# Performance work log

Measured on AMD Instinct MI355X. Metric: run time of the kernel, lower is better.

The kernel has to match this reference:

```python
import jax, jax.numpy as jnp
import numpy as np

N, D, H, K, L, C = 65536, 512, 256, 16, 3, 64  # n_support, embed_dim, D//2, max_clusters, num_levels, n_classes
EPS = 1e-5


def setup_inputs() -> dict:
    key = jax.random.key(0)
    ks = jax.random.split(key, 18)
    s = 0.02
    inp = {
        "support_features": jax.random.normal(ks[0], (N, D), jnp.float32),
        "support_labels": jax.random.randint(ks[1], (N,), 0, C),
        # cluster heads (per level): Linear(D,H) -> ReLU -> Linear(H,K) -> Softmax
        "ch_w1": jax.random.normal(ks[2], (L, D, H), jnp.float32) * s,
        "ch_b1": jnp.zeros((L, H), jnp.float32),
        "ch_w2": jax.random.normal(ks[3], (L, H, K), jnp.float32) * s,
        "ch_b2": jnp.zeros((L, K), jnp.float32),
        # prototype refiners (per level): Linear(D,D) -> LayerNorm -> ReLU -> Linear(D,D)
        "ref_w1": jax.random.normal(ks[4], (L, D, D), jnp.float32) * s,
        "ref_b1": jnp.zeros((L, D), jnp.float32),
        "ln_g": jnp.ones((L, D), jnp.float32),
        "ln_b": jnp.zeros((L, D), jnp.float32),
        "ref_w2": jax.random.normal(ks[5], (L, D, D), jnp.float32) * s,
        "ref_b2": jnp.zeros((L, D), jnp.float32),
        # hierarchy combiner: Linear(L*D, D) -> ReLU -> Linear(D, D)
        "comb_w1": jax.random.normal(ks[6], (L * D, D), jnp.float32) * s,
        "comb_b1": jnp.zeros((D,), jnp.float32),
        "comb_w2": jax.random.normal(ks[7], (D, D), jnp.float32) * s,
        "comb_b2": jnp.zeros((D,), jnp.float32),
    }
    return inp


def _layernorm(x, g, b):
    m = x.mean(-1, keepdims=True)
    v = ((x - m) ** 2).mean(-1, keepdims=True)
    return (x - m) * jax.lax.rsqrt(v + EPS) * g + b


def reference(support_features, support_labels, ch_w1, ch_b1, ch_w2, ch_b2,
              ref_w1, ref_b1, ln_g, ln_b, ref_w2, ref_b2,
              comb_w1, comb_b1, comb_w2, comb_b2):
    current = support_features  # [N, D]; per-class offsets applied via label gather
    level_protos = []
    for l in range(L):
        # cluster head; softmax omitted since argmax is softmax-invariant
        logits = jax.nn.relu(current @ ch_w1[l] + ch_b1[l]) @ ch_w2[l] + ch_b2[l]  # [N, K]
        assign = jnp.argmax(logits, axis=-1)  # [N]
        seg = support_labels * K + assign  # combined (class, cluster) segment id
        sums = jax.ops.segment_sum(current, seg, num_segments=C * K)  # [C*K, D]
        cnt = jax.ops.segment_sum(jnp.ones((N,), current.dtype), seg, num_segments=C * K)
        means = sums / jnp.maximum(cnt, 1.0)[:, None]  # empty clusters -> 0, masked below
        h = means @ ref_w1[l] + ref_b1[l]
        h = jax.nn.relu(_layernorm(h, ln_g[l], ln_b[l]))
        refined = (h @ ref_w2[l] + ref_b2[l]).reshape(C, K, D)
        ne = (cnt.reshape(C, K) > 0).astype(current.dtype)  # non-empty cluster mask
        lp = (refined * ne[..., None]).sum(1) / ne.sum(1)[:, None]  # [C, D] mean over non-empty
        level_protos.append(lp)
        current = current + lp[support_labels]
    combined = jnp.concatenate(level_protos, axis=-1)  # [C, L*D]
    protos = jax.nn.relu(combined @ comb_w1 + comb_b1) @ comb_w2 + comb_b2  # [C, D]
    return protos
```

## Files before the change

kernel.cpp:

```cpp
#include <hip/hip_runtime.h>

#define NPTS 65536
#define DIM  512
#define HID  256
#define KCL  16
#define NLVL 3
#define NCLS 64
#define NSEG (NCLS*KCL)
#define EPSF 1e-5f

typedef __bf16 bf16_t;
typedef bf16_t bf16x4 __attribute__((ext_vector_type(4)));
typedef bf16_t bf16x8 __attribute__((ext_vector_type(8)));
typedef float  f32x4  __attribute__((ext_vector_type(4)));

#define LDA 40
#define LDH2 68

__global__ __launch_bounds__(256) void wsplit_kernel(
    const float* __restrict__ w1, bf16_t* __restrict__ hiT, bf16_t* __restrict__ loT)
{
  int gid = blockIdx.x * 256 + threadIdx.x;
  int n = gid >> 9, k = gid & 511;
  int l = n >> 8, j = n & 255;
  float v = w1[l*DIM*HID + k*HID + j];
  bf16_t h = (bf16_t)v;
  hiT[gid] = h;
  loT[gid] = (bf16_t)(v - (float)h);
}

__global__ __launch_bounds__(256) void wsplit2_kernel(
    const float* __restrict__ w1, const float* __restrict__ w2,
    bf16_t* __restrict__ h1, bf16_t* __restrict__ l1,
    bf16_t* __restrict__ h2, bf16_t* __restrict__ l2)
{
  const int per = NLVL*DIM*DIM;
  int gid = blockIdx.x * 256 + threadIdx.x;
  const float* w = (gid < per) ? w1 : w2;
  bf16_t* hh = (gid < per) ? h1 : h2;
  bf16_t* ll = (gid < per) ? l1 : l2;
  int g2 = (gid < per) ? gid : gid - per;
  int n512 = g2 >> 9, k = g2 & 511;
  int l = n512 >> 9, n = n512 & 511;
  float v = w[(size_t)l*DIM*DIM + (size_t)k*DIM + n];
  bf16_t h = (bf16_t)v;
  hh[g2] = h;
  ll[g2] = (bf16_t)(v - (float)h);
}

__global__ __launch_bounds__(256) void wsplitW2_kernel(
    const float* __restrict__ w2, bf16_t* __restrict__ hiT, bf16_t* __restrict__ loT)
{
  int gid = blockIdx.x * 256 + threadIdx.x;
  int l = gid >> 12, rem = gid & 4095;
  int k2 = rem >> 8, k = rem & 255;
  float v = w2[(size_t)l*HID*KCL + k*KCL + k2];
  bf16_t h = (bf16_t)v;
  hiT[gid] = h;
  loT[gid] = (bf16_t)(v - (float)h);
}

__global__ __launch_bounds__(512, 4) void gemmassign_kernel(
    const float* __restrict__ feat,
    const bf16_t* __restrict__ BhiT, const bf16_t* __restrict__ BloT,
    const bf16_t* __restrict__ w2hT, const bf16_t* __restrict__ w2lT,
    const float* __restrict__ offsrc, int ldo,
    const int* __restrict__ labels,
    const float* __restrict__ pb2,
    int* __restrict__ asg, int* __restrict__ cnt)
{
  __shared__ __align__(16) unsigned char SMraw[768*LDA*2];
  __shared__ int labs[128];
  bf16_t* SM  = (bf16_t*)SMraw;
  bf16_t* Ahi = SM;
  bf16_t* Alo = SM + 128*LDA;
  bf16_t* Bhi = SM + 256*LDA;
  bf16_t* Blo = SM + 512*LDA;

  const int t = threadIdx.x;
  const int row0 = blockIdx.x * 128;
  const int w = t >> 6, lane = t & 63;
  const int wm = w & 1, wn = w >> 1;
  const int fm = lane & 15, fq = lane >> 4;

  if (t < 128) labs[t] = labels[row0 + t];
  const float pv = pb2[fm];

  f32x4 acc[4][4];
  #pragma unroll
  for (int i = 0; i < 4; i++)
    #pragma unroll
    for (int j = 0; j < 4; j++)
      #pragma unroll
      for (int r = 0; r < 4; r++) acc[i][j][r] = 0.f;

  for (int kc = 0; kc < DIM; kc += 32) {
    __syncthreads();
    #pragma unroll
    for (int p = 0; p < 2; p++) {
      int idx = t + 512*p;
      int r = idx >> 3, c = idx & 7;
      float4 v = *(const float4*)&feat[(size_t)(row0 + r)*DIM + kc + c*4];
      bf16x4 hi, lo;
      hi[0] = (bf16_t)v.x; lo[0] = (bf16_t)(v.x - (float)hi[0]);
      hi[1] = (bf16_t)v.y; lo[1] = (bf16_t)(v.y - (float)hi[1]);
      hi[2] = (bf16_t)v.z; lo[2] = (bf16_t)(v.z - (float)hi[2]);
      hi[3] = (bf16_t)v.w; lo[3] = (bf16_t)(v.w - (float)hi[3]);
      *(bf16x4*)&Ahi[r*LDA + c*4] = hi;
      *(bf16x4*)&Alo[r*LDA + c*4] = lo;
    }
    #pragma unroll
    for (int p = 0; p < 2; p++) {
      int idx = t + 512*p;
      int n = idx >> 2, c = idx & 3;
      *(bf16x8*)&Bhi[n*LDA + c*8] = *(const bf16x8*)&BhiT[(size_t)n*DIM + kc + c*8];
      *(bf16x8*)&Blo[n*LDA + c*8] = *(const bf16x8*)&BloT[(size_t)n*DIM + kc + c*8];
    }
    __syncthreads();

    bf16x8 ah[4], al[4], bh[4], bl[4];
    #pragma unroll
    for (int mt = 0; mt < 4; mt++) {
      int rr = (wm*64 + mt*16 + fm)*LDA + fq*8;
      ah[mt] = *(bf16x8*)&Ahi[rr];
      al[mt] = *(bf16x8*)&Alo[rr];
    }
    #pragma unroll
    for (int nt = 0; nt < 4; nt++) {
      int rr = (wn*64 + nt*16 + fm)*LDA + fq*8;
      bh[nt] = *(bf16x8*)&Bhi[rr];
      bl[nt] = *(bf16x8*)&Blo[rr];
    }
    #pragma unroll
    for (int mt = 0; mt < 4; mt++)
      #pragma unroll
      for (int nt = 0; nt < 4; nt++) {
        acc[mt][nt] = __builtin_amdgcn_mfma_f32_16x16x32_bf16(ah[mt], bh[nt], acc[mt][nt], 0, 0, 0);
        acc[mt][nt] = __builtin_amdgcn_mfma_f32_16x16x32_bf16(ah[mt], bl[nt], acc[mt][nt], 0, 0, 0);
        acc[mt][nt] = __builtin_amdgcn_mfma_f32_16x16x32_bf16(al[mt], bh[nt], acc[mt][nt], 0, 0, 0);
      }
  }

  __syncthreads();
  float* hS = (float*)SMraw;

  f32x4 lg = {0.f, 0.f, 0.f, 0.f};

  #pragma unroll
  for (int q = 0; q < 4; q++) {
    if (wn == q) {
      #pragma unroll
      for (int nt = 0; nt < 4; nt++) {
        int colq = nt*16 + fm;
        int colg = q*64 + colq;
        #pragma unroll
        for (int mt = 0; mt < 4; mt++)
          #pragma unroll
          for (int r = 0; r < 4; r++) {
            int row = wm*64 + mt*16 + fq*4 + r;
            float hv = fmaxf(acc[mt][nt][r] +
                             offsrc[(size_t)labs[row]*ldo + colg], 0.f);
            hS[row*LDH2 + colq] = hv;
          }
      }
    }
    __syncthreads();

    #pragma unroll
    for (int s = 0; s < 2; s++) {
      int kb = s*32 + fq*8;
      f32x4 a0 = *(f32x4*)&hS[(w*16 + fm)*LDH2 + kb];
      f32x4 a1 = *(f32x4*)&hS[(w*16 + fm)*LDH2 + kb + 4];
      bf16x8 ahf, alf;
      #pragma unroll
      for (int j = 0; j < 4; j++) {
        bf16_t h0 = (bf16_t)a0[j]; ahf[j]   = h0; alf[j]   = (bf16_t)(a0[j] - (float)h0);
        bf16_t h1 = (bf16_t)a1[j]; ahf[4+j] = h1; alf[4+j] = (bf16_t)(a1[j] - (float)h1);
      }
      bf16x8 bhf = *(const bf16x8*)&w2hT[fm*HID + q*64 + kb];
      bf16x8 blf = *(const bf16x8*)&w2lT[fm*HID + q*64 + kb];
      lg = __builtin_amdgcn_mfma_f32_16x16x32_bf16(ahf, bhf, lg, 0, 0, 0);
      lg = __builtin_amdgcn_mfma_f32_16x16x32_bf16(ahf, blf, lg, 0, 0, 0);
      lg = __builtin_amdgcn_mfma_f32_16x16x32_bf16(alf, bhf, lg, 0, 0, 0);
    }
    __syncthreads();
  }

  #pragma unroll
  for (int r = 0; r < 4; r++) {
    float v = lg[r] + pv;
    int idx = fm;
    #pragma unroll
    for (int ofs = 8; ofs > 0; ofs >>= 1) {
      float ov = __shfl_xor(v, ofs, 16);
      int   oi = __shfl_xor(idx, ofs, 16);
      if (ov > v || (ov == v && oi < idx)) { v = ov; idx = oi; }
    }
    if (fm == 0) {
      int rloc = w*16 + fq*4 + r;
      asg[row0 + rloc] = idx;
      atomicAdd(&cnt[labs[rloc]*KCL + idx], 1);
    }
  }
}

__global__ __launch_bounds__(256) void gemm64_kernel(
    const float* __restrict__ Asrc,
    const bf16_t* __restrict__ BhiT, const bf16_t* __restrict__ BloT,
    float* __restrict__ C, int mode,
    const int* __restrict__ cnt, const float* __restrict__ off,
    const float* __restrict__ b1, const float* __restrict__ g,
    const float* __restrict__ bb,
    const float* __restrict__ mS, const float* __restrict__ rS)
{
  __shared__ __align__(16) bf16_t Ahi[64*LDA];
  __shared__ __align__(16) bf16_t Alo[64*LDA];
  __shared__ __align__(16) bf16_t Bhi[64*LDA];
  __shared__ __align__(16) bf16_t Blo[64*LDA];
  __shared__ float rm[64], rr_[64];

  const int t = threadIdx.x;
  const int row0 = blockIdx.x * 64, col0 = blockIdx.y * 64;
  const int w = t >> 6, lane = t & 63;
  const int wm = w & 1, wn = w >> 1;
  const int fm = lane & 15, fq = lane >> 4;

  if (t < 64) {
    if (mode == 1) {
      int n = cnt[row0 + t];
      rm[t] = (float)n;
      rr_[t] = 1.f / fmaxf((float)n, 1.f);
    } else {
      rm[t] = mS[row0 + t];
      rr_[t] = rS[row0 + t];
    }
  }

  f32x4 acc[2][2];
  #pragma unroll
  for (int i = 0; i < 2; i++)
    #pragma unroll
    for (int j = 0; j < 2; j++)
      #pragma unroll
      for (int r = 0; r < 4; r++) acc[i][j][r] = 0.f;

  for (int kc = 0; kc < DIM; kc += 32) {
    __syncthreads();
    #pragma unroll
    for (int p = 0; p < 2; p++) {
      int idx = t + 256*p;
      int r = idx >> 3, c = idx & 7;
      float4 v = *(const float4*)&Asrc[(size_t)(row0 + r)*DIM + kc + c*4];
      if (mode == 1) {
        int cls = (row0 + r) >> 4;
        float4 o = *(const float4*)&off[(size_t)cls*DIM + kc + c*4];
        float n = rm[r], inv = rr_[r];
        v.x = (v.x + n*o.x) * inv; v.y = (v.y + n*o.y) * inv;
        v.z = (v.z + n*o.z) * inv; v.w = (v.w + n*o.w) * inv;
      } else {
        float4 B1 = *(const float4*)&b1[kc + c*4];
        float4 G4 = *(const float4*)&g[kc + c*4];
        float4 BB = *(const float4*)&bb[kc + c*4];
        float m = rm[r], rs = rr_[r];
        v.x = fmaxf((v.x + B1.x - m)*rs*G4.x + BB.x, 0.f);
        v.y = fmaxf((v.y + B1.y - m)*rs*G4.y + BB.y, 0.f);
        v.z = fmaxf((v.z + B1.z - m)*rs*G4.z + BB.z, 0.f);
        v.w = fmaxf((v.w + B1.w - m)*rs*G4.w + BB.w, 0.f);
      }
      bf16x4 hi, lo;
      hi[0] = (bf16_t)v.x; lo[0] = (bf16_t)(v.x - (float)hi[0]);
      hi[1] = (bf16_t)v.y; lo[1] = (bf16_t)(v.y - (float)hi[1]);
      hi[2] = (bf16_t)v.z; lo[2] = (bf16_t)(v.z - (float)hi[2]);
      hi[3] = (bf16_t)v.w; lo[3] = (bf16_t)(v.w - (float)hi[3]);
      *(bf16x4*)&Ahi[r*LDA + c*4] = hi;
      *(bf16x4*)&Alo[r*LDA + c*4] = lo;
    }
    {
      int n = t >> 2, kof = (t & 3)*8;
      *(bf16x8*)&Bhi[n*LDA + kof] = *(const bf16x8*)&BhiT[(size_t)(col0 + n)*DIM + kc + kof];
      *(bf16x8*)&Blo[n*LDA + kof] = *(const bf16x8*)&BloT[(size_t)(col0 + n)*DIM + kc + kof];
    }
    __syncthreads();

    bf16x8 ah[2], al[2], bh[2], bl[2];
    #pragma unroll
    for (int mt = 0; mt < 2; mt++) {
      int idx = (wm*32 + mt*16 + fm)*LDA + fq*8;
      ah[mt] = *(bf16x8*)&Ahi[idx];
      al[mt] = *(bf16x8*)&Alo[idx];
    }
    #pragma unroll
    for (int nt = 0; nt < 2; nt++) {
      int idx = (wn*32 + nt*16 + fm)*LDA + fq*8;
      bh[nt] = *(bf16x8*)&Bhi[idx];
      bl[nt] = *(bf16x8*)&Blo[idx];
    }
    #pragma unroll
    for (int mt = 0; mt < 2; mt++)
      #pragma unroll
      for (int nt = 0; nt < 2; nt++) {
        acc[mt][nt] = __builtin_amdgcn_mfma_f32_16x16x32_bf16(ah[mt], bh[nt], acc[mt][nt], 0, 0, 0);
        acc[mt][nt] = __builtin_amdgcn_mfma_f32_16x16x32_bf16(ah[mt], bl[nt], acc[mt][nt], 0, 0, 0);
        acc[mt][nt] = __builtin_amdgcn_mfma_f32_16x16x32_bf16(al[mt], bh[nt], acc[mt][nt], 0, 0, 0);
        acc[mt][nt] = __builtin_amdgcn_mfma_f32_16x16x32_bf16(al[mt], bl[nt], acc[mt][nt], 0, 0, 0);
      }
  }

  #pragma unroll
  for (int mt = 0; mt < 2; mt++)
    #pragma unroll
    for (int nt = 0; nt < 2; nt++) {
      int col = col0 + wn*32 + nt*16 + fm;
      int rowb = row0 + wm*32 + mt*16 + fq*4;
      #pragma unroll
      for (int r = 0; r < 4; r++)
        C[(size_t)(rowb + r)*DIM + col] = acc[mt][nt][r];
    }
}

__global__ __launch_bounds__(256) void lnstats_kernel(
    const float* __restrict__ Y1, const float* __restrict__ b1,
    float* __restrict__ mS, float* __restrict__ rS)
{
  int r = blockIdx.x, t = threadIdx.x;
  float x0 = Y1[(size_t)r*DIM + t]       + b1[t];
  float x1 = Y1[(size_t)r*DIM + t + 256] + b1[t + 256];
  float s1 = x0 + x1, s2 = x0*x0 + x1*x1;
  #pragma unroll
  for (int ofs = 32; ofs > 0; ofs >>= 1) {
    s1 += __shfl_xor(s1, ofs);
    s2 += __shfl_xor(s2, ofs);
  }
  __shared__ float r1[4], r2[4];
  int lane = t & 63, w = t >> 6;
  if (lane == 0) { r1[w] = s1; r2[w] = s2; }
  __syncthreads();
  if (t == 0) {
    s1 = r1[0] + r1[1] + r1[2] + r1[3];
    s2 = r2[0] + r2[1] + r2[2] + r2[3];
    float m = s1 * (1.f/512.f);
    float var = s2 * (1.f/512.f) - m*m;
    mS[r] = m;
    rS[r] = rsqrtf(var + EPSF);
  }
}

__global__ __launch_bounds__(256) void protoOffgemm_kernel(
    const float* __restrict__ Y2, const float* __restrict__ b2,
    const int* __restrict__ cnt, float* __restrict__ off, float* __restrict__ lp_out,
    const float* __restrict__ w1next, const float* __restrict__ b1next,
    float* __restrict__ offW1b)
{
  __shared__ float offs[DIM];
  int c = blockIdx.x, t = threadIdx.x;
  int nes = 0;
  #pragma unroll
  for (int k = 0; k < KCL; k++) nes += (cnt[c*KCL + k] > 0);
  float inv = 1.f / (float)nes;
  #pragma unroll
  for (int h = 0; h < 2; h++) {
    int d = t + h*256;
    float s = 0.f;
    #pragma unroll
    for (int k = 0; k < KCL; k++)
      if (cnt[c*KCL + k] > 0) s += Y2[(size_t)(c*KCL + k)*DIM + d];
    float lp = s * inv + b2[d];
    lp_out[c*DIM + d] = lp;
    float on = off[c*DIM + d] + lp;
    off[c*DIM + d] = on;
    offs[d] = on;
  }
  if (w1next == nullptr) return;
  __syncthreads();
  float a = 0.f;
  #pragma unroll 4
  for (int d = 0; d < DIM; d++)
    a = fmaf(offs[d], w1next[d*HID + t], a);
  offW1b[c*HID + t] = a + b1next[t];
}

__global__ void scan_kernel(const int* __restrict__ cnt, int* __restrict__ seg_st,
                            int* __restrict__ cursor)
{
  int t = threadIdx.x;
  int4 v = *(const int4*)&cnt[t*4];
  int a0 = v.x, a1 = v.x + v.y, a2 = a1 + v.z, tot = a2 + v.w;
  int lane = t & 63, w = t >> 6;
  int sc = tot;
  #pragma unroll
  for (int ofs = 1; ofs < 64; ofs <<= 1) {
    int u = __shfl_up(sc, ofs);
    if (lane >= ofs) sc += u;
  }
  __shared__ int wt[4];
  if (lane == 63) wt[w] = sc;
  __syncthreads();
  int base = 0;
  #pragma unroll
  for (int i = 0; i < 4; i++) if (i < w) base += wt[i];
  int excl = base + sc - tot;
  seg_st[t*4 + 1] = excl + a0;
  seg_st[t*4 + 2] = excl + a1;
  seg_st[t*4 + 3] = excl + a2;
  seg_st[t*4 + 4] = excl + tot;
  if (t == 0) seg_st[0] = 0;
  int4 cur = {excl, excl + a0, excl + a1, excl + a2};
  *(int4*)&cursor[t*4] = cur;
}

__global__ __launch_bounds__(256) void scatter_kernel(
    const int* __restrict__ labels, const int* __restrict__ asg,
    int* __restrict__ cursor, int* __restrict__ rowlist, int* __restrict__ seglist)
{
  int i = blockIdx.x * 256 + threadIdx.x;
  int seg = labels[i]*KCL + asg[i];
  int pos = atomicAdd(&cursor[seg], 1);
  rowlist[pos] = i;
  seglist[pos] = seg;
}

__global__ __launch_bounds__(256) void means3_kernel(
    const float* __restrict__ feat, const int* __restrict__ rowlist,
    const int* __restrict__ seglist, float* __restrict__ sums)
{
  __shared__ int rows[64];
  __shared__ int segs[65];
  int t = threadIdx.x;
  int i0 = blockIdx.x * 64;
  int col = blockIdx.y * 256 + t;
  if (t < 64) { rows[t] = rowlist[i0 + t]; segs[t] = seglist[i0 + t]; }
  if (t == 64) segs[64] = -1;
  __syncthreads();
  float acc = 0.f;
  for (int base = 0; base < 64; base += 16) {
    float v[16];
    #pragma unroll
    for (int j = 0; j < 16; j++)
      v[j] = feat[(size_t)rows[base + j]*DIM + col];
    #pragma unroll
    for (int j = 0; j < 16; j++) {
      acc += v[j];
      if (segs[base + j] != segs[base + j + 1]) {
        atomicAdd(&sums[(size_t)segs[base + j]*DIM + col], acc);
        acc = 0.f;
      }
    }
  }
}

__global__ __launch_bounds__(256) void fgemm1_kernel(
    const float* __restrict__ lp_all, const float* __restrict__ cw1,
    float* __restrict__ Hacc)
{
  __shared__ float As[64*132];
  __shared__ float Ws[128*64];
  int t = threadIdx.x;
  int nc = blockIdx.x * 64, kc = blockIdx.y * 128;

  #pragma unroll
  for (int p = 0; p < 8; p++) {
    int i = t + 256*p;
    int m = i >> 5, k0 = (i & 31) << 2;
    int k = kc + k0;
    int l = k >> 9, d = k & 511;
    *(float4*)&As[m*132 + k0] = *(const float4*)&lp_all[(size_t)(l*NCLS + m)*DIM + d];
  }
  #pragma unroll
  for (int p = 0; p < 8; p++) {
    int i = t + 256*p;
    int k = i >> 4, n0 = (i & 15) << 2;
    *(float4*)&Ws[k*64 + n0] = *(const float4*)&cw1[(size_t)(kc + k)*DIM + nc + n0];
  }
  __syncthreads();

  int tn = (t & 15) * 4, tmg = (t >> 4) * 4;
  float acc[4][4];
  #pragma unroll
  for (int i = 0; i < 4; i++)
    #pragma unroll
    for (int j = 0; j < 4; j++) acc[i][j] = 0.f;

  for (int k = 0; k < 128; k += 4) {
    float4 a[4], w[4];
    #pragma unroll
    for (int i = 0; i < 4; i++) a[i] = *(float4*)&As[(tmg + i)*132 + k];
    #pragma unroll
    for (int j = 0; j < 4; j++) w[j] = *(float4*)&Ws[(k + j)*64 + tn];
    #pragma unroll
    for (int kk = 0; kk < 4; kk++) {
      float wv[4] = {w[kk].x, w[kk].y, w[kk].z, w[kk].w};
      float av[4] = {a[0][kk], a[1][kk], a[2][kk], a[3][kk]};
      #pragma unroll
      for (int i = 0; i < 4; i++)
        #pragma unroll
        for (int j = 0; j < 4; j++)
          acc[i][j] = fmaf(av[i], wv[j], acc[i][j]);
    }
  }
  #pragma unroll
  for (int i = 0; i < 4; i++)
    #pragma unroll
    for (int j = 0; j < 4; j++)
      atomicAdd(&Hacc[(size_t)(tmg + i)*DIM + nc + tn + j], acc[i][j]);
}

__global__ __launch_bounds__(256) void fgemm2_kernel(
    const float* __restrict__ Hacc, const float* __restrict__ cb1,
    const float* __restrict__ cw2, float* __restrict__ Oacc)
{
  __shared__ float As[64*132];
  __shared__ float Ws[128*64];
  int t = threadIdx.x;
  int nc = blockIdx.x * 64, kc = blockIdx.y * 128;

  #pragma unroll
  for (int p = 0; p < 8; p++) {
    int i = t + 256*p;
    int m = i >> 5, k0 = (i & 31) << 2;
    float4 v = *(const float4*)&Hacc[(size_t)m*DIM + kc + k0];
    float4 b = *(const float4*)&cb1[kc + k0];
    v.x = fmaxf(v.x + b.x, 0.f); v.y = fmaxf(v.y + b.y, 0.f);
    v.z = fmaxf(v.z + b.z, 0.f); v.w = fmaxf(v.w + b.w, 0.f);
    *(float4*)&As[m*132 + k0] = v;
  }
  #pragma unroll
  for (int p = 0; p < 8; p++) {
    int i = t + 256*p;
    int k = i >> 4, n0 = (i & 15) << 2;
    *(float4*)&Ws[k*64 + n0] = *(const float4*)&cw2[(size_t)(kc + k)*DIM + nc + n0];
  }
  __syncthreads();

  int tn = (t & 15) * 4, tmg = (t >> 4) * 4;
  float acc[4][4];
  #pragma unroll
  for (int i = 0; i < 4; i++)
    #pragma unroll
    for (int j = 0; j < 4; j++) acc[i][j] = 0.f;

  for (int k = 0; k < 128; k += 4) {
    float4 a[4], w[4];
    #pragma unroll
    for (int i = 0; i < 4; i++) a[i] = *(float4*)&As[(tmg + i)*132 + k];
    #pragma unroll
    for (int j = 0; j < 4; j++) w[j] = *(float4*)&Ws[(k + j)*64 + tn];
    #pragma unroll
    for (int kk = 0; kk < 4; kk++) {
      float wv[4] = {w[kk].x, w[kk].y, w[kk].z, w[kk].w};
      float av[4] = {a[0][kk], a[1][kk], a[2][kk], a[3][kk]};
      #pragma unroll
      for (int i = 0; i < 4; i++)
        #pragma unroll
        for (int j = 0; j < 4; j++)
          acc[i][j] = fmaf(av[i], wv[j], acc[i][j]);
    }
  }
  #pragma unroll
  for (int i = 0; i < 4; i++)
    #pragma unroll
    for (int j = 0; j < 4; j++)
      atomicAdd(&Oacc[(size_t)(tmg + i)*DIM + nc + tn + j], acc[i][j]);
}

__global__ __launch_bounds__(256) void fbias_kernel(
    const float* __restrict__ Oacc, const float* __restrict__ cb2,
    float* __restrict__ out)
{
  int gi = blockIdx.x * 256 + threadIdx.x;
  out[gi] = Oacc[gi] + cb2[gi & 511];
}

extern "C" void kernel_launch(void* const* d_in, const int* in_sizes, int n_in,
                              void* d_out, int out_size, void* d_ws, size_t ws_size,
                              hipStream_t stream) {
  const float* feat   = (const float*)d_in[0];
  const int*   labels = (const int*)d_in[1];
  const float* ch_w1  = (const float*)d_in[2];
  const float* ch_b1  = (const float*)d_in[3];
  const float* ch_w2  = (const float*)d_in[4];
  const float* ch_b2  = (const float*)d_in[5];
  const float* ref_w1 = (const float*)d_in[6];
  const float* ref_b1 = (const float*)d_in[7];
  const float* ln_g   = (const float*)d_in[8];
  const float* ln_b   = (const float*)d_in[9];
  const float* ref_w2 = (const float*)d_in[10];
  const float* ref_b2 = (const float*)d_in[11];
  const float* cw1    = (const float*)d_in[12];
  const float* cb1    = (const float*)d_in[13];
  const float* cw2    = (const float*)d_in[14];
  const float* cb2    = (const float*)d_in[15];
  float* out = (float*)d_out;

  float* wsf = (float*)d_ws;
  float* off    = wsf;
  float* lp_all = off + 32768;
  float* sums   = lp_all + 98304;
  int*   cnt_i  = (int*)(sums + 524288);
  float* offW1b = sums + 524288 + 1024;
  float* Hacc   = offW1b + 16384;
  float* Oacc   = Hacc + 32768;
  float* Y1     = Oacc + 32768;
  float* Y2     = Y1 + 524288;
  float* mS     = Y2 + 524288;
  float* rS     = mS + 1024;

  bf16_t* whiT  = (bf16_t*)(rS + 1024);
  bf16_t* wloT  = whiT + (size_t)NLVL*HID*DIM;
  bf16_t* r1hiT = wloT + (size_t)NLVL*HID*DIM;
  bf16_t* r1loT = r1hiT + (size_t)NLVL*DIM*DIM;
  bf16_t* r2hiT = r1loT + (size_t)NLVL*DIM*DIM;
  bf16_t* r2loT = r2hiT + (size_t)NLVL*DIM*DIM;
  int* asg     = (int*)(r2loT + (size_t)NLVL*DIM*DIM);
  int* rowlist = asg + NPTS;
  int* seglist = rowlist + NPTS;
  int* seg_st  = seglist + NPTS;
  int* cursor  = seg_st + 1040;
  bf16_t* w2hT = (bf16_t*)(cursor + NSEG);
  bf16_t* w2lT = w2hT + (size_t)NLVL*KCL*HID;

  hipMemsetAsync(off, 0, NCLS*DIM*sizeof(float), stream);

  wsplit_kernel<<<NLVL*HID*DIM/256, 256, 0, stream>>>(ch_w1, whiT, wloT);
  wsplit2_kernel<<<2*NLVL*DIM*DIM/256, 256, 0, stream>>>(
      ref_w1, ref_w2, r1hiT, r1loT, r2hiT, r2loT);
  wsplitW2_kernel<<<NLVL*KCL*HID/256, 256, 0, stream>>>(ch_w2, w2hT, w2lT);

  for (int l = 0; l < NLVL; l++) {
    hipMemsetAsync(sums, 0, (NSEG*DIM + NSEG)*sizeof(float), stream);

    const float* offsrc = (l == 0) ? ch_b1 : offW1b;
    int ldo = (l == 0) ? 0 : HID;

    gemmassign_kernel<<<NPTS/128, 512, 0, stream>>>(
        feat, whiT + (size_t)l*HID*DIM, wloT + (size_t)l*HID*DIM,
        w2hT + (size_t)l*KCL*HID, w2lT + (size_t)l*KCL*HID,
        offsrc, ldo, labels,
        ch_b2 + (size_t)l*KCL,
        asg, cnt_i);

    scan_kernel<<<1, 256, 0, stream>>>(cnt_i, seg_st, cursor);

    scatter_kernel<<<NPTS/256, 256, 0, stream>>>(labels, asg, cursor, rowlist, seglist);

    means3_kernel<<<dim3(NPTS/64, DIM/256), 256, 0, stream>>>(
        feat, rowlist, seglist, sums);

    gemm64_kernel<<<dim3(NSEG/64, DIM/64), 256, 0, stream>>>(
        sums, r1hiT + (size_t)l*DIM*DIM, r1loT + (size_t)l*DIM*DIM, Y1, 1,
        cnt_i, off, nullptr, nullptr, nullptr, nullptr, nullptr);

    lnstats_kernel<<<NSEG, 256, 0, stream>>>(
        Y1, ref_b1 + (size_t)l*DIM, mS, rS);

    gemm64_kernel<<<dim3(NSEG/64, DIM/64), 256, 0, stream>>>(
        Y1, r2hiT + (size_t)l*DIM*DIM, r2loT + (size_t)l*DIM*DIM, Y2, 2,
        nullptr, nullptr, ref_b1 + (size_t)l*DIM,
        ln_g + (size_t)l*DIM, ln_b + (size_t)l*DIM, mS, rS);

    protoOffgemm_kernel<<<NCLS, 256, 0, stream>>>(
        Y2, ref_b2 + (size_t)l*DIM, cnt_i, off, lp_all + (size_t)l*NCLS*DIM,
        (l < NLVL-1) ? (ch_w1 + (size_t)(l+1)*DIM*HID) : nullptr,
        (l < NLVL-1) ? (ch_b1 + (size_t)(l+1)*HID) : nullptr,
        offW1b);
  }

  hipMemsetAsync(Hacc, 0, 2*NCLS*DIM*sizeof(float), stream);
  fgemm1_kernel<<<dim3(DIM/64, NLVL*DIM/128), 256, 0, stream>>>(lp_all, cw1, Hacc);
  fgemm2_kernel<<<dim3(DIM/64, DIM/128), 256, 0, stream>>>(Hacc, cb1, cw2, Oacc);
  fbias_kernel<<<NCLS*DIM/256, 256, 0, stream>>>(Oacc, cb2, out);
}
```

Before: 838.3 us.

## Fuse LayerNorm stats into first refiner GEMM and double-buffer hidden tile

The separate LayerNorm statistics kernel is removed. The first refiner GEMM epilogue now accumulates per-row sum and sum-of-squares with shuffles and atomics, and the second GEMM derives mean and rstd from them. In the assignment kernel the hidden-activation staging now uses two shared buffers, so writing the next quarter overlaps reading the current one and a barrier per quarter is dropped. The protoOffgemm dot product is also split into four accumulators for more ILP. Costs are larger LDS use (which may lower occupancy), atomics, and a one-pass variance formula that can be less numerically stable.

```diff
diff --git a/kernel.cpp b/kernel.cpp
--- a/kernel.cpp
+++ b/kernel.cpp
@@ -69,7 +69,7 @@
     const float* __restrict__ pb2,
     int* __restrict__ asg, int* __restrict__ cnt)
 {
-  __shared__ __align__(16) unsigned char SMraw[768*LDA*2];
+  __shared__ __align__(16) unsigned char SMraw[2*128*LDH2*4];
   __shared__ int labs[128];
   bf16_t* SM  = (bf16_t*)SMraw;
   bf16_t* Ahi = SM;
@@ -142,35 +142,40 @@
   }
 
   __syncthreads();
-  float* hS = (float*)SMraw;
+  float* hA = (float*)SMraw;
+  float* hB = hA + 128*LDH2;
+
+  auto writeQ = [&](int q, float* buf) {
+    #pragma unroll
+    for (int nt = 0; nt < 4; nt++) {
+      int colq = nt*16 + fm;
+      int colg = q*64 + colq;
+      #pragma unroll
+      for (int mt = 0; mt < 4; mt++)
+        #pragma unroll
+        for (int r = 0; r < 4; r++) {
+          int row = wm*64 + mt*16 + fq*4 + r;
+          buf[row*LDH2 + colq] =
+              fmaxf(acc[mt][nt][r] + offsrc[(size_t)labs[row]*ldo + colg], 0.f);
+        }
+    }
+  };
 
   f32x4 lg = {0.f, 0.f, 0.f, 0.f};
 
+  if (wn == 0) writeQ(0, hA);
+  __syncthreads();
   #pragma unroll
   for (int q = 0; q < 4; q++) {
-    if (wn == q) {
-      #pragma unroll
-      for (int nt = 0; nt < 4; nt++) {
-        int colq = nt*16 + fm;
-        int colg = q*64 + colq;
-        #pragma unroll
-        for (int mt = 0; mt < 4; mt++)
-          #pragma unroll
-          for (int r = 0; r < 4; r++) {
-            int row = wm*64 + mt*16 + fq*4 + r;
-            float hv = fmaxf(acc[mt][nt][r] +
-                             offsrc[(size_t)labs[row]*ldo + colg], 0.f);
-            hS[row*LDH2 + colq] = hv;
-          }
-      }
-    }
-    __syncthreads();
+    float* cur = (q & 1) ? hB : hA;
+    float* nxt = (q & 1) ? hA : hB;
+    if (q < 3 && wn == q + 1) writeQ(q + 1, nxt);
 
     #pragma unroll
     for (int s = 0; s < 2; s++) {
       int kb = s*32 + fq*8;
-      f32x4 a0 = *(f32x4*)&hS[(w*16 + fm)*LDH2 + kb];
-      f32x4 a1 = *(f32x4*)&hS[(w*16 + fm)*LDH2 + kb + 4];
+      f32x4 a0 = *(f32x4*)&cur[(w*16 + fm)*LDH2 + kb];
+      f32x4 a1 = *(f32x4*)&cur[(w*16 + fm)*LDH2 + kb + 4];
       bf16x8 ahf, alf;
       #pragma unroll
       for (int j = 0; j < 4; j++) {
@@ -183,7 +188,7 @@
       lg = __builtin_amdgcn_mfma_f32_16x16x32_bf16(ahf, blf, lg, 0, 0, 0);
       lg = __builtin_amdgcn_mfma_f32_16x16x32_bf16(alf, bhf, lg, 0, 0, 0);
     }
-    __syncthreads();
+    if (q < 3) __syncthreads();
   }
 
   #pragma unroll
@@ -210,8 +215,7 @@
     float* __restrict__ C, int mode,
     const int* __restrict__ cnt, const float* __restrict__ off,
     const float* __restrict__ b1, const float* __restrict__ g,
-    const float* __restrict__ bb,
-    const float* __restrict__ mS, const float* __restrict__ rS)
+    const float* __restrict__ bb, float* __restrict__ mP)
 {
   __shared__ __align__(16) bf16_t Ahi[64*LDA];
   __shared__ __align__(16) bf16_t Alo[64*LDA];
@@ -231,8 +235,11 @@
       rm[t] = (float)n;
       rr_[t] = 1.f / fmaxf((float)n, 1.f);
     } else {
-      rm[t] = mS[row0 + t];
-      rr_[t] = rS[row0 + t];
+      float s1 = mP[row0 + t], s2 = mP[NSEG + row0 + t];
+      float m = s1 * (1.f/512.f);
+      float var = s2 * (1.f/512.f) - m*m;
+      rm[t] = m;
+      rr_[t] = rsqrtf(var + EPSF);
     }
   }
 
@@ -316,32 +323,32 @@
       for (int r = 0; r < 4; r++)
         C[(size_t)(rowb + r)*DIM + col] = acc[mt][nt][r];
     }
-}
-
-__global__ __launch_bounds__(256) void lnstats_kernel(
-    const float* __restrict__ Y1, const float* __restrict__ b1,
-    float* __restrict__ mS, float* __restrict__ rS)
-{
-  int r = blockIdx.x, t = threadIdx.x;
-  float x0 = Y1[(size_t)r*DIM + t]       + b1[t];
-  float x1 = Y1[(size_t)r*DIM + t + 256] + b1[t + 256];
-  float s1 = x0 + x1, s2 = x0*x0 + x1*x1;
-  #pragma unroll
-  for (int ofs = 32; ofs > 0; ofs >>= 1) {
-    s1 += __shfl_xor(s1, ofs);
-    s2 += __shfl_xor(s2, ofs);
-  }
-  __shared__ float r1[4], r2[4];
-  int lane = t & 63, w = t >> 6;
-  if (lane == 0) { r1[w] = s1; r2[w] = s2; }
-  __syncthreads();
-  if (t == 0) {
-    s1 = r1[0] + r1[1] + r1[2] + r1[3];
-    s2 = r2[0] + r2[1] + r2[2] + r2[3];
-    float m = s1 * (1.f/512.f);
-    float var = s2 * (1.f/512.f) - m*m;
-    mS[r] = m;
-    rS[r] = rsqrtf(var + EPSF);
+
+  if (mode == 1) {
+    float b1v[2];
+    #pragma unroll
+    for (int nt = 0; nt < 2; nt++) b1v[nt] = b1[col0 + wn*32 + nt*16 + fm];
+    #pragma unroll
+    for (int mt = 0; mt < 2; mt++)
+      #pragma unroll
+      for (int r = 0; r < 4; r++) {
+        float c1 = 0.f, c2 = 0.f;
+        #pragma unroll
+        for (int nt = 0; nt < 2; nt++) {
+          float v = acc[mt][nt][r] + b1v[nt];
+          c1 += v; c2 += v*v;
+        }
+        #pragma unroll
+        for (int ofs = 8; ofs > 0; ofs >>= 1) {
+          c1 += __shfl_xor(c1, ofs, 16);
+          c2 += __shfl_xor(c2, ofs, 16);
+        }
+        if (fm == 0) {
+          int row = row0 + wm*32 + mt*16 + fq*4 + r;
+          atomicAdd(&mP[row], c1);
+          atomicAdd(&mP[NSEG + row], c2);
+        }
+      }
   }
 }
 
@@ -372,11 +379,15 @@
   }
   if (w1next == nullptr) return;
   __syncthreads();
-  float a = 0.f;
+  float a0 = 0.f, a1 = 0.f, a2 = 0.f, a3 = 0.f;
   #pragma unroll 4
-  for (int d = 0; d < DIM; d++)
-    a = fmaf(offs[d], w1next[d*HID + t], a);
-  offW1b[c*HID + t] = a + b1next[t];
+  for (int d = 0; d < DIM; d += 4) {
+    a0 = fmaf(offs[d+0], w1next[(d+0)*HID + t], a0);
+    a1 = fmaf(offs[d+1], w1next[(d+1)*HID + t], a1);
+    a2 = fmaf(offs[d+2], w1next[(d+2)*HID + t], a2);
+    a3 = fmaf(offs[d+3], w1next[(d+3)*HID + t], a3);
+  }
+  offW1b[c*HID + t] = ((a0 + a1) + (a2 + a3)) + b1next[t];
 }
 
 __global__ void scan_kernel(const int* __restrict__ cnt, int* __restrict__ seg_st,
@@ -596,27 +607,26 @@
   float* lp_all = off + 32768;
   float* sums   = lp_all + 98304;
   int*   cnt_i  = (int*)(sums + 524288);
-  float* offW1b = sums + 524288 + 1024;
+  float* mP     = (float*)(cnt_i + NSEG);
+  float* offW1b = mP + 2*NSEG;
   float* Hacc   = offW1b + 16384;
   float* Oacc   = Hacc + 32768;
   float* Y1     = Oacc + 32768;
   float* Y2     = Y1 + 524288;
-  float* mS     = Y2 + 524288;
-  float* rS     = mS + 1024;
-
-  bf16_t* whiT  = (bf16_t*)(rS + 1024);
+
+  bf16_t* whiT  = (bf16_t*)(Y2 + 524288);
   bf16_t* wloT  = whiT + (size_t)NLVL*HID*DIM;
   bf16_t* r1hiT = wloT + (size_t)NLVL*HID*DIM;
   bf16_t* r1loT = r1hiT + (size_t)NLVL*DIM*DIM;
   bf16_t* r2hiT = r1loT + (size_t)NLVL*DIM*DIM;
   bf16_t* r2loT = r2hiT + (size_t)NLVL*DIM*DIM;
-  int* asg     = (int*)(r2loT + (size_t)NLVL*DIM*DIM);
+  bf16_t* w2hT  = r2loT + (size_t)NLVL*DIM*DIM;
+  bf16_t* w2lT  = w2hT + (size_t)NLVL*KCL*HID;
+  int* asg     = (int*)(w2lT + (size_t)NLVL*KCL*HID);
   int* rowlist = asg + NPTS;
   int* seglist = rowlist + NPTS;
   int* seg_st  = seglist + NPTS;
   int* cursor  = seg_st + 1040;
-  bf16_t* w2hT = (bf16_t*)(cursor + NSEG);
-  bf16_t* w2lT = w2hT + (size_t)NLVL*KCL*HID;
 
   hipMemsetAsync(off, 0, NCLS*DIM*sizeof(float), stream);
 
@@ -626,7 +636,7 @@
   wsplitW2_kernel<<<NLVL*KCL*HID/256, 256, 0, stream>>>(ch_w2, w2hT, w2lT);
 
   for (int l = 0; l < NLVL; l++) {
-    hipMemsetAsync(sums, 0, (NSEG*DIM + NSEG)*sizeof(float), stream);
+    hipMemsetAsync(sums, 0, (NSEG*DIM + NSEG + 2*NSEG)*sizeof(float), stream);
 
     const float* offsrc = (l == 0) ? ch_b1 : offW1b;
     int ldo = (l == 0) ? 0 : HID;
@@ -647,15 +657,12 @@
 
     gemm64_kernel<<<dim3(NSEG/64, DIM/64), 256, 0, stream>>>(
         sums, r1hiT + (size_t)l*DIM*DIM, r1loT + (size_t)l*DIM*DIM, Y1, 1,
-        cnt_i, off, nullptr, nullptr, nullptr, nullptr, nullptr);
-
-    lnstats_kernel<<<NSEG, 256, 0, stream>>>(
-        Y1, ref_b1 + (size_t)l*DIM, mS, rS);
+        cnt_i, off, ref_b1 + (size_t)l*DIM, nullptr, nullptr, mP);
 
     gemm64_kernel<<<dim3(NSEG/64, DIM/64), 256, 0, stream>>>(
         Y1, r2hiT + (size_t)l*DIM*DIM, r2loT + (size_t)l*DIM*DIM, Y2, 2,
         nullptr, nullptr, ref_b1 + (size_t)l*DIM,
-        ln_g + (size_t)l*DIM, ln_b + (size_t)l*DIM, mS, rS);
+        ln_g + (size_t)l*DIM, ln_b + (size_t)l*DIM, mP);
 
     protoOffgemm_kernel<<<NCLS, 256, 0, stream>>>(
         Y2, ref_b2 + (size_t)l*DIM, cnt_i, off, lp_all + (size_t)l*NCLS*DIM,
```

After: 812.5 us. 1.03x faster.
